# Kernel optimization log

Hardware: AMD Instinct MI355X
Metric: run time of the kernel (lower is better)

Reference implementation:

```python
import jax, jax.numpy as jnp
import numpy as np

D_MODEL = 1024
N_HEADS = 16
D_K = D_MODEL // N_HEADS


def setup_inputs() -> dict:
    key = jax.random.key(0)
    ks = jax.random.split(key, 12)
    B, S = 4, 2048
    scale = 1.0 / np.sqrt(D_MODEL)
    inp = {
        "Q_in": jax.random.normal(ks[0], (B, S, D_MODEL), jnp.float32),
        "K_in": jax.random.normal(ks[1], (B, S, D_MODEL), jnp.float32),
        "V_in": jax.random.normal(ks[2], (B, S, D_MODEL), jnp.float32),
        "Wq": jax.random.normal(ks[3], (D_MODEL, D_MODEL), jnp.float32) * scale,
        "bq": jnp.zeros((D_MODEL,), jnp.float32),
        "Wk": jax.random.normal(ks[4], (D_MODEL, D_MODEL), jnp.float32) * scale,
        "bk": jnp.zeros((D_MODEL,), jnp.float32),
        "Wv": jax.random.normal(ks[5], (D_MODEL, D_MODEL), jnp.float32) * scale,
        "bv": jnp.zeros((D_MODEL,), jnp.float32),
        "Wo": jax.random.normal(ks[6], (D_MODEL, D_MODEL), jnp.float32) * scale,
        "bo": jnp.zeros((D_MODEL,), jnp.float32),
    }
    return inp


def reference(Q_in, K_in, V_in, Wq, bq, Wk, bk, Wv, bv, Wo, bo):
    B, S, _ = Q_in.shape
    # QKV projections, split into heads: [B, H, S, d_k]
    def proj(x, W, b):
        y = jnp.einsum('bsd,df->bsf', x, W) + b
        return y.reshape(B, S, N_HEADS, D_K).transpose(0, 2, 1, 3)

    Q = proj(Q_in, Wq, bq)
    K = proj(K_in, Wk, bk)
    V = proj(V_in, Wv, bv)

    # scaled dot-product attention (dropout is identity in eval)
    scores = jnp.einsum('bhqd,bhkd->bhqk', Q, K) / jnp.sqrt(jnp.float32(D_K)).astype(Q.dtype)
    p_attn = jax.nn.softmax(scores, axis=-1)
    x = jnp.einsum('bhqk,bhkd->bhqd', p_attn, V)

    # merge heads and output projection
    x = x.transpose(0, 2, 1, 3).reshape(B, S, D_MODEL)
    return jnp.einsum('bsd,df->bsf', x, Wo) + bo
```

## Files before the change

kernel.cpp:

```cpp
#include <hip/hip_runtime.h>

#define DEV __device__ __forceinline__

typedef _Float16 f16;
typedef __attribute__((ext_vector_type(8))) _Float16 f16x8;
typedef __attribute__((ext_vector_type(4))) _Float16 f16x4;
typedef __attribute__((ext_vector_type(2))) __fp16 fp16v2;
typedef __attribute__((ext_vector_type(4))) float floatx4;

constexpr int DMODEL = 1024;
constexpr int SLEN = 2048;
constexpr float SCALE_Q = 0.125f * 1.4426950408889634f;

DEV void gll16(const void* g, void* lds) {
    __builtin_amdgcn_global_load_lds((const __attribute__((address_space(1))) void*)g,
                                     (__attribute__((address_space(3))) void*)lds, 16, 0, 0);
}

#if __has_builtin(__builtin_amdgcn_exp2f)
DEV float fast_exp2(float x) { return __builtin_amdgcn_exp2f(x); }
#else
DEV float fast_exp2(float x) { return __expf(x * 0.6931471805599453f); }
#endif

DEV unsigned pkh2(float a, float b) {
    union { fp16v2 h; unsigned u; } c;
    c.h = __builtin_amdgcn_cvt_pkrtz(a, b);
    return c.u;
}

#if __has_builtin(__builtin_amdgcn_permlane32_swap) && __has_builtin(__builtin_amdgcn_permlane16_swap)
DEV void pl32swap(unsigned& x, unsigned& y) {
    auto r = __builtin_amdgcn_permlane32_swap(x, y, false, false);
    x = r[0]; y = r[1];
}
DEV void pl16swap(unsigned& x, unsigned& y) {
    auto r = __builtin_amdgcn_permlane16_swap(x, y, false, false);
    x = r[0]; y = r[1];
}
#else
DEV void pl32swap(unsigned& x, unsigned& y) {
    unsigned xs = (unsigned)__shfl_xor((int)x, 32, 64);
    unsigned ys = (unsigned)__shfl_xor((int)y, 32, 64);
    bool lo = (threadIdx.x & 63) < 32;
    unsigned nx = lo ? x : ys, ny = lo ? xs : y;
    x = nx; y = ny;
}
DEV void pl16swap(unsigned& x, unsigned& y) {
    unsigned xs = (unsigned)__shfl_xor((int)x, 16, 64);
    unsigned ys = (unsigned)__shfl_xor((int)y, 16, 64);
    bool ev = (((threadIdx.x & 63) >> 4) & 1) == 0;
    unsigned nx = ev ? x : ys, ny = ev ? xs : y;
    x = nx; y = ny;
}
#endif

DEV f16x8 xform(const floatx4& s0, const floatx4& s1) {
    unsigned X  = pkh2(fast_exp2(s0[0]), fast_exp2(s0[1]));
    unsigned Xp = pkh2(fast_exp2(s0[2]), fast_exp2(s0[3]));
    unsigned Y  = pkh2(fast_exp2(s1[0]), fast_exp2(s1[1]));
    unsigned Yp = pkh2(fast_exp2(s1[2]), fast_exp2(s1[3]));
    pl32swap(X, Y);  pl16swap(X, Y);
    pl32swap(Xp, Yp); pl16swap(Xp, Yp);
    union { unsigned u[4]; f16x8 v; } o;
    o.u[0] = X; o.u[1] = Xp; o.u[2] = Y; o.u[3] = Yp;
    return o.v;
}

__global__ void cvt3(const float* __restrict__ A0, const float* __restrict__ A1,
                     const float* __restrict__ A2, f16* __restrict__ O0,
                     f16* __restrict__ O1, f16* __restrict__ O2) {
    const int seg = blockIdx.x >> 12;
    const int i = (blockIdx.x & 4095) * 256 + threadIdx.x;
    const float* in = seg == 0 ? A0 : seg == 1 ? A1 : A2;
    f16* out = seg == 0 ? O0 : seg == 1 ? O1 : O2;
    const float4 a = ((const float4*)in)[2 * i];
    const float4 b = ((const float4*)in)[2 * i + 1];
    f16x8 h;
    h[0] = (f16)a.x; h[1] = (f16)a.y; h[2] = (f16)a.z; h[3] = (f16)a.w;
    h[4] = (f16)b.x; h[5] = (f16)b.y; h[6] = (f16)b.z; h[7] = (f16)b.w;
    ((f16x8*)out)[i] = h;
}

__global__ void wtrans4(const float* __restrict__ W0, const float* __restrict__ W1,
                        const float* __restrict__ W2, const float* __restrict__ W3,
                        f16* __restrict__ T0, f16* __restrict__ T1,
                        f16* __restrict__ T2, f16* __restrict__ T3) {
    __shared__ float t[32][33];
    const int w = blockIdx.x >> 10, bid = blockIdx.x & 1023;
    const float* W = w == 0 ? W0 : w == 1 ? W1 : w == 2 ? W2 : W3;
    f16* Wt = w == 0 ? T0 : w == 1 ? T1 : w == 2 ? T2 : T3;
    const int tn = bid & 31, tk = bid >> 5;
    const int c = threadIdx.x & 31, r0 = threadIdx.x >> 5;
    for (int i = 0; i < 4; ++i) {
        int r = r0 + i * 8;
        t[r][c] = W[(tk * 32 + r) * DMODEL + tn * 32 + c];
    }
    __syncthreads();
    for (int i = 0; i < 4; ++i) {
        int r = r0 + i * 8;
        Wt[(tn * 32 + r) * DMODEL + tk * 32 + c] = (f16)t[c][r];
    }
}

__global__ __launch_bounds__(256, 3)
void gemm_qkv(const f16* __restrict__ A0, const f16* __restrict__ A1, const f16* __restrict__ A2,
              const f16* __restrict__ B0, const f16* __restrict__ B1, const f16* __restrict__ B2,
              const float* __restrict__ bi0, const float* __restrict__ bi1, const float* __restrict__ bi2,
              f16* __restrict__ C0, f16* __restrict__ C1, f16* __restrict__ C2, int epi_base) {
    __shared__ f16 As[128 * 32];
    __shared__ f16 Bs[128 * 32];
    const int seg = blockIdx.x >> 9, inner = blockIdx.x & 511;
    const int epi = epi_base + seg;
    const f16* A = seg == 0 ? A0 : seg == 1 ? A1 : A2;
    const f16* Bt = seg == 0 ? B0 : seg == 1 ? B1 : B2;
    const float* bias = seg == 0 ? bi0 : seg == 1 ? bi1 : bi2;
    f16* Cp = seg == 0 ? C0 : seg == 1 ? C1 : C2;

    const int tid = threadIdx.x;
    const int wid = tid >> 6, lane = tid & 63;
    const int quad = lane >> 4, l16 = lane & 15;
    const int bm = inner & 63, bn = inner >> 6;
    const int row0 = bm * 128, col0 = bn * 128;
    const int wm = (wid >> 1) * 64, wn = (wid & 1) * 64;

    floatx4 acc[4][4];
    for (int i = 0; i < 4; ++i)
        for (int j = 0; j < 4; ++j) acc[i][j] = {0.f, 0.f, 0.f, 0.f};

    for (int k0 = 0; k0 < DMODEL; k0 += 32) {
        __syncthreads();
        for (int j = 0; j < 2; ++j) {
            int off = (j * 4 + wid) * 1024 + lane * 16;
            int r = off >> 6, cb = (off & 63) >> 1;
            gll16(Bt + (col0 + r) * DMODEL + k0 + cb, (char*)Bs + (j * 4 + wid) * 1024);
            gll16(A + (row0 + r) * DMODEL + k0 + cb, (char*)As + (j * 4 + wid) * 1024);
        }
        __syncthreads();

        f16x8 af[4], bf[4];
        for (int mi = 0; mi < 4; ++mi)
            af[mi] = *(const f16x8*)&As[(wm + mi * 16 + l16) * 32 + quad * 8];
        for (int ni = 0; ni < 4; ++ni)
            bf[ni] = *(const f16x8*)&Bs[(wn + ni * 16 + l16) * 32 + quad * 8];
        for (int mi = 0; mi < 4; ++mi)
            for (int ni = 0; ni < 4; ++ni)
                acc[mi][ni] = __builtin_amdgcn_mfma_f32_16x16x32_f16(af[mi], bf[ni], acc[mi][ni], 0, 0, 0);
    }

    const float scale = (epi == 0) ? SCALE_Q : 1.0f;
    for (int mi = 0; mi < 4; ++mi) {
        for (int ni = 0; ni < 4; ++ni) {
            const int gr0 = row0 + wm + mi * 16 + quad * 4;
            const int gc = col0 + wn + ni * 16 + l16;
            const float bv = bias[gc];
            if (epi == 2) {
                const int b_ = gr0 >> 11, s0 = gr0 & 2047;
                const int h_ = gc >> 6, d_ = gc & 63;
                const int bh = b_ * 16 + h_;
                const int csw = ((s0 >> 3) & 15) ^ (d_ & 7);
                const int s0w = (s0 & ~127) | (csw << 3) | (s0 & 7);
                f16x4 o;
                for (int r = 0; r < 4; ++r) o[r] = (f16)(acc[mi][ni][r] + bv);
                *(f16x4*)&Cp[(bh * 64 + d_) * SLEN + s0w] = o;
            } else {
                for (int r = 0; r < 4; ++r) {
                    const int gr = gr0 + r;
                    const int b_ = gr >> 11, s_ = gr & 2047;
                    const int h_ = gc >> 6, d_ = gc & 63;
                    const int bh = b_ * 16 + h_;
                    const int dsw = (((d_ >> 3) ^ (s_ & 7)) << 3) | (d_ & 7);
                    Cp[(bh * SLEN + s_) * 64 + dsw] = (f16)((acc[mi][ni][r] + bv) * scale);
                }
            }
        }
    }
}

__global__ __launch_bounds__(256, 3)
void gemm_out(const f16* __restrict__ A, const f16* __restrict__ Bt,
              const float* __restrict__ bias, float* __restrict__ Cp) {
    __shared__ f16 As[128 * 32];
    __shared__ f16 Bs[128 * 32];
    const int tid = threadIdx.x;
    const int wid = tid >> 6, lane = tid & 63;
    const int quad = lane >> 4, l16 = lane & 15;
    const int bm = blockIdx.x & 63, bn = blockIdx.x >> 6;
    const int row0 = bm * 128, col0 = bn * 128;
    const int wm = (wid >> 1) * 64, wn = (wid & 1) * 64;

    floatx4 acc[4][4];
    for (int i = 0; i < 4; ++i)
        for (int j = 0; j < 4; ++j) acc[i][j] = {0.f, 0.f, 0.f, 0.f};

    for (int k0 = 0; k0 < DMODEL; k0 += 32) {
        __syncthreads();
        for (int j = 0; j < 2; ++j) {
            int off = (j * 4 + wid) * 1024 + lane * 16;
            int r = off >> 6, cb = (off & 63) >> 1;
            gll16(Bt + (col0 + r) * DMODEL + k0 + cb, (char*)Bs + (j * 4 + wid) * 1024);
            gll16(A + (row0 + r) * DMODEL + k0 + cb, (char*)As + (j * 4 + wid) * 1024);
        }
        __syncthreads();

        f16x8 af[4], bf[4];
        for (int mi = 0; mi < 4; ++mi)
            af[mi] = *(const f16x8*)&As[(wm + mi * 16 + l16) * 32 + quad * 8];
        for (int ni = 0; ni < 4; ++ni)
            bf[ni] = *(const f16x8*)&Bs[(wn + ni * 16 + l16) * 32 + quad * 8];
        for (int mi = 0; mi < 4; ++mi)
            for (int ni = 0; ni < 4; ++ni)
                acc[mi][ni] = __builtin_amdgcn_mfma_f32_16x16x32_f16(af[mi], bf[ni], acc[mi][ni], 0, 0, 0);
    }

    for (int mi = 0; mi < 4; ++mi)
        for (int ni = 0; ni < 4; ++ni) {
            const int gr0 = row0 + wm + mi * 16 + quad * 4;
            const int gc = col0 + wn + ni * 16 + l16;
            const float bv = bias[gc];
            for (int r = 0; r < 4; ++r)
                Cp[(gr0 + r) * DMODEL + gc] = acc[mi][ni][r] + bv;
        }
}

__global__ __launch_bounds__(256, 4)
void flash_k(const f16* __restrict__ Qh, const f16* __restrict__ Kh,
             const f16* __restrict__ Vt, f16* __restrict__ attn) {
    __shared__ f16 smem[16384];
    f16* Qs = smem;
    f16* Ks = smem;
    f16* Vs = smem + 8192;

    const int tid = threadIdx.x;
    const int wid = tid >> 6, lane = tid & 63;
    const int quad = lane >> 4, l16 = lane & 15;
    const int xcd = blockIdx.x & 7, jj = blockIdx.x >> 3;
    const int bh = xcd * 8 + (jj & 7), qt = jj >> 3;
    const int mq = wid * 32;

    const f16* Qbase = Qh + (bh * SLEN + qt * 128) * 64;
#pragma unroll
    for (int j = 0; j < 4; ++j) {
        const int ch = j * 4 + wid;
        gll16(Qbase + ch * 512 + lane * 8, (char*)Qs + ch * 1024);
    }
    __syncthreads();

    f16x8 qf[2][2];
#pragma unroll
    for (int nq = 0; nq < 2; ++nq)
#pragma unroll
        for (int kc = 0; kc < 2; ++kc)
            qf[nq][kc] = *(const f16x8*)&Qs[(mq + nq * 16 + l16) * 64 +
                                            (((kc * 4 + quad) ^ (l16 & 7)) << 3)];

    floatx4 oacc[2][5];
    for (int nq = 0; nq < 2; ++nq)
        for (int md = 0; md < 5; ++md) oacc[nq][md] = {0.f, 0.f, 0.f, 0.f};

    const f16x8 ones = {(f16)1, (f16)1, (f16)1, (f16)1, (f16)1, (f16)1, (f16)1, (f16)1};
    const f16* Kb = Kh + bh * SLEN * 64;
    const f16* Vb = Vt + bh * 64 * SLEN;

    for (int kv0 = 0; kv0 < SLEN; kv0 += 128) {
        __syncthreads();
#pragma unroll
        for (int j = 0; j < 4; ++j) {
            const int ch = j * 4 + wid;
            gll16(Kb + kv0 * 64 + ch * 512 + lane * 8, (char*)Ks + ch * 1024);
        }
#pragma unroll
        for (int j = 0; j < 4; ++j) {
            const int ch = j * 4 + wid;
            const int ci = ch * 64 + lane;
            const int d_ = ci >> 4, o_ = (ci & 15) * 8;
            gll16(Vb + d_ * SLEN + kv0 + o_, (char*)Vs + ch * 1024);
        }
        __syncthreads();

        f16x8 pf[2];
#pragma unroll
        for (int c = 0; c < 4; ++c) {
            floatx4 sacc[2][2];
            for (int nq = 0; nq < 2; ++nq)
                for (int t = 0; t < 2; ++t) sacc[nq][t] = {0.f, 0.f, 0.f, 0.f};
#pragma unroll
            for (int t = 0; t < 2; ++t) {
                const int a = c * 2 + t;
#pragma unroll
                for (int kc = 0; kc < 2; ++kc) {
                    f16x8 kf = *(const f16x8*)&Ks[(a * 16 + l16) * 64 +
                                                  (((kc * 4 + quad) ^ (l16 & 7)) << 3)];
                    for (int nq = 0; nq < 2; ++nq)
                        sacc[nq][t] = __builtin_amdgcn_mfma_f32_16x16x32_f16(
                            kf, qf[nq][kc], sacc[nq][t], 0, 0, 0);
                }
            }
            if (c > 0) {
                const int cp = c - 1;
#pragma unroll
                for (int md = 0; md < 4; ++md) {
                    f16x8 vf = *(const f16x8*)&Vs[(md * 16 + l16) * 128 +
                                                  (((cp * 4 + quad) ^ (l16 & 7)) << 3)];
                    for (int nq = 0; nq < 2; ++nq)
                        oacc[nq][md] = __builtin_amdgcn_mfma_f32_16x16x32_f16(
                            vf, pf[nq], oacc[nq][md], 0, 0, 0);
                }
                for (int nq = 0; nq < 2; ++nq)
                    oacc[nq][4] = __builtin_amdgcn_mfma_f32_16x16x32_f16(
                        ones, pf[nq], oacc[nq][4], 0, 0, 0);
            }
#pragma unroll
            for (int nq = 0; nq < 2; ++nq) pf[nq] = xform(sacc[nq][0], sacc[nq][1]);
        }
#pragma unroll
        for (int md = 0; md < 4; ++md) {
            f16x8 vf = *(const f16x8*)&Vs[(md * 16 + l16) * 128 +
                                          (((3 * 4 + quad) ^ (l16 & 7)) << 3)];
            for (int nq = 0; nq < 2; ++nq)
                oacc[nq][md] = __builtin_amdgcn_mfma_f32_16x16x32_f16(
                    vf, pf[nq], oacc[nq][md], 0, 0, 0);
        }
        for (int nq = 0; nq < 2; ++nq)
            oacc[nq][4] = __builtin_amdgcn_mfma_f32_16x16x32_f16(
                ones, pf[nq], oacc[nq][4], 0, 0, 0);
    }

    const int b_ = bh >> 4, h_ = bh & 15;
#pragma unroll
    for (int nq = 0; nq < 2; ++nq) {
        const float linv = __frcp_rn(oacc[nq][4][0]);
        const int tok = b_ * SLEN + qt * 128 + mq + nq * 16 + l16;
#pragma unroll
        for (int md = 0; md < 4; ++md) {
            f16x4 o;
            for (int r = 0; r < 4; ++r) o[r] = (f16)(oacc[nq][md][r] * linv);
            *(f16x4*)&attn[tok * DMODEL + h_ * 64 + md * 16 + quad * 4] = o;
        }
    }
}

extern "C" void kernel_launch(void* const* d_in, const int* in_sizes, int n_in,
                              void* d_out, int out_size, void* d_ws, size_t ws_size,
                              hipStream_t stream) {
    (void)in_sizes; (void)n_in; (void)out_size;
    const float* Q_in = (const float*)d_in[0];
    const float* K_in = (const float*)d_in[1];
    const float* V_in = (const float*)d_in[2];
    const float* Wq = (const float*)d_in[3];
    const float* bq = (const float*)d_in[4];
    const float* Wk = (const float*)d_in[5];
    const float* bk = (const float*)d_in[6];
    const float* Wv = (const float*)d_in[7];
    const float* bv = (const float*)d_in[8];
    const float* Wo = (const float*)d_in[9];
    const float* bo = (const float*)d_in[10];
    float* out = (float*)d_out;

    char* ws = (char*)d_ws;
    const size_t MB = 1u << 20;
    f16* wtq = (f16*)(ws + 0 * MB);
    f16* wtk = (f16*)(ws + 2 * MB);
    f16* wtv = (f16*)(ws + 4 * MB);
    f16* wto = (f16*)(ws + 6 * MB);
    f16* Qh  = (f16*)(ws + 8 * MB);
    f16* Kh  = (f16*)(ws + 24 * MB);
    f16* Vt  = (f16*)(ws + 40 * MB);
    f16* At  = (f16*)(ws + 56 * MB);

    wtrans4<<<4096, 256, 0, stream>>>(Wq, Wk, Wv, Wo, wtq, wtk, wtv, wto);

    if (ws_size >= 120 * MB) {
        f16* Ac0 = (f16*)(ws + 72 * MB);
        f16* Ac1 = (f16*)(ws + 88 * MB);
        f16* Ac2 = (f16*)(ws + 104 * MB);
        cvt3<<<3 * 4096, 256, 0, stream>>>(Q_in, K_in, V_in, Ac0, Ac1, Ac2);
        gemm_qkv<<<1536, 256, 0, stream>>>(Ac0, Ac1, Ac2, wtq, wtk, wtv,
                                           bq, bk, bv, Qh, Kh, Vt, 0);
    } else {
        f16* Ac = At;
        cvt3<<<4096, 256, 0, stream>>>(Q_in, Q_in, Q_in, Ac, Ac, Ac);
        gemm_qkv<<<512, 256, 0, stream>>>(Ac, Ac, Ac, wtq, wtq, wtq, bq, bq, bq,
                                          Qh, Qh, Qh, 0);
        cvt3<<<4096, 256, 0, stream>>>(K_in, K_in, K_in, Ac, Ac, Ac);
        gemm_qkv<<<512, 256, 0, stream>>>(Ac, Ac, Ac, wtk, wtk, wtk, bk, bk, bk,
                                          Kh, Kh, Kh, 1);
        cvt3<<<4096, 256, 0, stream>>>(V_in, V_in, V_in, Ac, Ac, Ac);
        gemm_qkv<<<512, 256, 0, stream>>>(Ac, Ac, Ac, wtv, wtv, wtv, bv, bv, bv,
                                          Vt, Vt, Vt, 2);
    }

    flash_k<<<1024, 256, 0, stream>>>(Qh, Kh, Vt, At);
    gemm_out<<<512, 256, 0, stream>>>(At, wto, bo, out);
}
```

Measured before the change: 348.6 us.

## Double-buffer GEMM and flash-attention loads and enlarge attention query tile

Moves the shared GEMM main loop into a helper that double-buffers A/B tiles in LDS, prefetching the next k-slice with global_load_lds while computing on the current one, using vmcnt waits and raw barriers. The flash-attention kernel likewise double-buffers its K/V tiles. It also doubles the query rows per block to 256, with 64 per wave, so each loaded K/V tile is reused across more queries, and it halves the grid. This hides global load latency and cuts K/V traffic, but doubles LDS use and raises register pressure, which lowers occupancy (launch bounds drop to 2) and leaves fewer blocks to spread across the device.

```diff
diff --git a/kernel.cpp b/kernel.cpp
--- a/kernel.cpp
+++ b/kernel.cpp
@@ -103,40 +103,36 @@
     }
 }
 
-__global__ __launch_bounds__(256, 3)
-void gemm_qkv(const f16* __restrict__ A0, const f16* __restrict__ A1, const f16* __restrict__ A2,
-              const f16* __restrict__ B0, const f16* __restrict__ B1, const f16* __restrict__ B2,
-              const float* __restrict__ bi0, const float* __restrict__ bi1, const float* __restrict__ bi2,
-              f16* __restrict__ C0, f16* __restrict__ C1, f16* __restrict__ C2, int epi_base) {
-    __shared__ f16 As[128 * 32];
-    __shared__ f16 Bs[128 * 32];
-    const int seg = blockIdx.x >> 9, inner = blockIdx.x & 511;
-    const int epi = epi_base + seg;
-    const f16* A = seg == 0 ? A0 : seg == 1 ? A1 : A2;
-    const f16* Bt = seg == 0 ? B0 : seg == 1 ? B1 : B2;
-    const float* bias = seg == 0 ? bi0 : seg == 1 ? bi1 : bi2;
-    f16* Cp = seg == 0 ? C0 : seg == 1 ? C1 : C2;
-
-    const int tid = threadIdx.x;
+DEV void gemm_core(const f16* __restrict__ A, const f16* __restrict__ Bt,
+                   f16* smem, int row0, int col0, int tid, floatx4 (&acc)[4][4]) {
     const int wid = tid >> 6, lane = tid & 63;
     const int quad = lane >> 4, l16 = lane & 15;
-    const int bm = inner & 63, bn = inner >> 6;
-    const int row0 = bm * 128, col0 = bn * 128;
     const int wm = (wid >> 1) * 64, wn = (wid & 1) * 64;
-
-    floatx4 acc[4][4];
-    for (int i = 0; i < 4; ++i)
-        for (int j = 0; j < 4; ++j) acc[i][j] = {0.f, 0.f, 0.f, 0.f};
-
-    for (int k0 = 0; k0 < DMODEL; k0 += 32) {
-        __syncthreads();
-        for (int j = 0; j < 2; ++j) {
-            int off = (j * 4 + wid) * 1024 + lane * 16;
-            int r = off >> 6, cb = (off & 63) >> 1;
-            gll16(Bt + (col0 + r) * DMODEL + k0 + cb, (char*)Bs + (j * 4 + wid) * 1024);
-            gll16(A + (row0 + r) * DMODEL + k0 + cb, (char*)As + (j * 4 + wid) * 1024);
-        }
-        __syncthreads();
+    const int off = wid * 1024 + lane * 16;
+    const int r = off >> 6, cb = (off & 63) >> 1;
+
+    {
+        gll16(Bt + (col0 + r) * DMODEL + cb, (char*)(smem + 4096) + wid * 1024);
+        gll16(Bt + (col0 + r + 64) * DMODEL + cb, (char*)(smem + 4096) + 4096 + wid * 1024);
+        gll16(A + (row0 + r) * DMODEL + cb, (char*)smem + wid * 1024);
+        gll16(A + (row0 + r + 64) * DMODEL + cb, (char*)smem + 4096 + wid * 1024);
+    }
+    for (int it = 0; it < 32; ++it) {
+        f16* As = smem + (it & 1) * 8192;
+        f16* Bs = As + 4096;
+        if (it < 31) {
+            const int k0 = (it + 1) * 32;
+            f16* An = smem + ((it + 1) & 1) * 8192;
+            f16* Bn = An + 4096;
+            gll16(Bt + (col0 + r) * DMODEL + k0 + cb, (char*)Bn + wid * 1024);
+            gll16(Bt + (col0 + r + 64) * DMODEL + k0 + cb, (char*)Bn + 4096 + wid * 1024);
+            gll16(A + (row0 + r) * DMODEL + k0 + cb, (char*)An + wid * 1024);
+            gll16(A + (row0 + r + 64) * DMODEL + k0 + cb, (char*)An + 4096 + wid * 1024);
+            __builtin_amdgcn_s_waitcnt(0xF74);
+        } else {
+            __builtin_amdgcn_s_waitcnt(0xF70);
+        }
+        __builtin_amdgcn_s_barrier();
 
         f16x8 af[4], bf[4];
         for (int mi = 0; mi < 4; ++mi)
@@ -146,7 +142,35 @@
         for (int mi = 0; mi < 4; ++mi)
             for (int ni = 0; ni < 4; ++ni)
                 acc[mi][ni] = __builtin_amdgcn_mfma_f32_16x16x32_f16(af[mi], bf[ni], acc[mi][ni], 0, 0, 0);
-    }
+        __builtin_amdgcn_s_barrier();
+    }
+}
+
+__global__ __launch_bounds__(256, 3)
+void gemm_qkv(const f16* __restrict__ A0, const f16* __restrict__ A1, const f16* __restrict__ A2,
+              const f16* __restrict__ B0, const f16* __restrict__ B1, const f16* __restrict__ B2,
+              const float* __restrict__ bi0, const float* __restrict__ bi1, const float* __restrict__ bi2,
+              f16* __restrict__ C0, f16* __restrict__ C1, f16* __restrict__ C2, int epi_base) {
+    __shared__ f16 smem[16384];
+    const int seg = blockIdx.x >> 9, inner = blockIdx.x & 511;
+    const int epi = epi_base + seg;
+    const f16* A = seg == 0 ? A0 : seg == 1 ? A1 : A2;
+    const f16* Bt = seg == 0 ? B0 : seg == 1 ? B1 : B2;
+    const float* bias = seg == 0 ? bi0 : seg == 1 ? bi1 : bi2;
+    f16* Cp = seg == 0 ? C0 : seg == 1 ? C1 : C2;
+
+    const int tid = threadIdx.x;
+    const int wid = tid >> 6, lane = tid & 63;
+    const int quad = lane >> 4, l16 = lane & 15;
+    const int bm = inner & 63, bn = inner >> 6;
+    const int row0 = bm * 128, col0 = bn * 128;
+    const int wm = (wid >> 1) * 64, wn = (wid & 1) * 64;
+
+    floatx4 acc[4][4];
+    for (int i = 0; i < 4; ++i)
+        for (int j = 0; j < 4; ++j) acc[i][j] = {0.f, 0.f, 0.f, 0.f};
+
+    gemm_core(A, Bt, smem, row0, col0, tid, acc);
 
     const float scale = (epi == 0) ? SCALE_Q : 1.0f;
     for (int mi = 0; mi < 4; ++mi) {
@@ -180,8 +204,7 @@
 __global__ __launch_bounds__(256, 3)
 void gemm_out(const f16* __restrict__ A, const f16* __restrict__ Bt,
               const float* __restrict__ bias, float* __restrict__ Cp) {
-    __shared__ f16 As[128 * 32];
-    __shared__ f16 Bs[128 * 32];
+    __shared__ f16 smem[16384];
     const int tid = threadIdx.x;
     const int wid = tid >> 6, lane = tid & 63;
     const int quad = lane >> 4, l16 = lane & 15;
@@ -193,25 +216,7 @@
     for (int i = 0; i < 4; ++i)
         for (int j = 0; j < 4; ++j) acc[i][j] = {0.f, 0.f, 0.f, 0.f};
 
-    for (int k0 = 0; k0 < DMODEL; k0 += 32) {
-        __syncthreads();
-        for (int j = 0; j < 2; ++j) {
-            int off = (j * 4 + wid) * 1024 + lane * 16;
-            int r = off >> 6, cb = (off & 63) >> 1;
-            gll16(Bt + (col0 + r) * DMODEL + k0 + cb, (char*)Bs + (j * 4 + wid) * 1024);
-            gll16(A + (row0 + r) * DMODEL + k0 + cb, (char*)As + (j * 4 + wid) * 1024);
-        }
-        __syncthreads();
-
-        f16x8 af[4], bf[4];
-        for (int mi = 0; mi < 4; ++mi)
-            af[mi] = *(const f16x8*)&As[(wm + mi * 16 + l16) * 32 + quad * 8];
-        for (int ni = 0; ni < 4; ++ni)
-            bf[ni] = *(const f16x8*)&Bs[(wn + ni * 16 + l16) * 32 + quad * 8];
-        for (int mi = 0; mi < 4; ++mi)
-            for (int ni = 0; ni < 4; ++ni)
-                acc[mi][ni] = __builtin_amdgcn_mfma_f32_16x16x32_f16(af[mi], bf[ni], acc[mi][ni], 0, 0, 0);
-    }
+    gemm_core(A, Bt, smem, row0, col0, tid, acc);
 
     for (int mi = 0; mi < 4; ++mi)
         for (int ni = 0; ni < 4; ++ni) {
@@ -223,77 +228,87 @@
         }
 }
 
-__global__ __launch_bounds__(256, 4)
+__global__ __launch_bounds__(256, 2)
 void flash_k(const f16* __restrict__ Qh, const f16* __restrict__ Kh,
              const f16* __restrict__ Vt, f16* __restrict__ attn) {
-    __shared__ f16 smem[16384];
-    f16* Qs = smem;
-    f16* Ks = smem;
-    f16* Vs = smem + 8192;
-
+    __shared__ f16 smem[32768];
     const int tid = threadIdx.x;
     const int wid = tid >> 6, lane = tid & 63;
     const int quad = lane >> 4, l16 = lane & 15;
     const int xcd = blockIdx.x & 7, jj = blockIdx.x >> 3;
     const int bh = xcd * 8 + (jj & 7), qt = jj >> 3;
-    const int mq = wid * 32;
-
-    const f16* Qbase = Qh + (bh * SLEN + qt * 128) * 64;
-#pragma unroll
-    for (int j = 0; j < 4; ++j) {
+    const int wq = wid * 64;
+
+    f16* Qs = smem + 16384;
+    const f16* Qbase = Qh + (bh * SLEN + qt * 256) * 64;
+#pragma unroll
+    for (int j = 0; j < 8; ++j) {
         const int ch = j * 4 + wid;
         gll16(Qbase + ch * 512 + lane * 8, (char*)Qs + ch * 1024);
     }
     __syncthreads();
 
-    f16x8 qf[2][2];
-#pragma unroll
-    for (int nq = 0; nq < 2; ++nq)
+    f16x8 qf[4][2];
+#pragma unroll
+    for (int nq = 0; nq < 4; ++nq)
 #pragma unroll
         for (int kc = 0; kc < 2; ++kc)
-            qf[nq][kc] = *(const f16x8*)&Qs[(mq + nq * 16 + l16) * 64 +
+            qf[nq][kc] = *(const f16x8*)&Qs[(wq + nq * 16 + l16) * 64 +
                                             (((kc * 4 + quad) ^ (l16 & 7)) << 3)];
-
-    floatx4 oacc[2][5];
-    for (int nq = 0; nq < 2; ++nq)
+    __syncthreads();
+
+    floatx4 oacc[4][5];
+    for (int nq = 0; nq < 4; ++nq)
         for (int md = 0; md < 5; ++md) oacc[nq][md] = {0.f, 0.f, 0.f, 0.f};
 
     const f16x8 ones = {(f16)1, (f16)1, (f16)1, (f16)1, (f16)1, (f16)1, (f16)1, (f16)1};
     const f16* Kb = Kh + bh * SLEN * 64;
     const f16* Vb = Vt + bh * 64 * SLEN;
 
-    for (int kv0 = 0; kv0 < SLEN; kv0 += 128) {
-        __syncthreads();
-#pragma unroll
-        for (int j = 0; j < 4; ++j) {
-            const int ch = j * 4 + wid;
-            gll16(Kb + kv0 * 64 + ch * 512 + lane * 8, (char*)Ks + ch * 1024);
-        }
-#pragma unroll
-        for (int j = 0; j < 4; ++j) {
-            const int ch = j * 4 + wid;
-            const int ci = ch * 64 + lane;
-            const int d_ = ci >> 4, o_ = (ci & 15) * 8;
-            gll16(Vb + d_ * SLEN + kv0 + o_, (char*)Vs + ch * 1024);
-        }
-        __syncthreads();
-
-        f16x8 pf[2];
+#pragma unroll
+    for (int j = 0; j < 4; ++j) {
+        const int ch = j * 4 + wid;
+        gll16(Kb + ch * 512 + lane * 8, (char*)smem + ch * 1024);
+        const int ci = ch * 64 + lane;
+        gll16(Vb + (ci >> 4) * SLEN + (ci & 15) * 8, (char*)(smem + 8192) + ch * 1024);
+    }
+
+    for (int t = 0; t < 16; ++t) {
+        f16* Ks = smem + (t & 1) * 16384;
+        f16* Vs = Ks + 8192;
+        if (t < 15) {
+            const int kv0n = (t + 1) * 128;
+            f16* Kn = smem + ((t + 1) & 1) * 16384;
+            f16* Vn = Kn + 8192;
+#pragma unroll
+            for (int j = 0; j < 4; ++j) {
+                const int ch = j * 4 + wid;
+                gll16(Kb + kv0n * 64 + ch * 512 + lane * 8, (char*)Kn + ch * 1024);
+                const int ci = ch * 64 + lane;
+                gll16(Vb + (ci >> 4) * SLEN + kv0n + (ci & 15) * 8, (char*)Vn + ch * 1024);
+            }
+            __builtin_amdgcn_s_waitcnt(0xF78);
+        } else {
+            __builtin_amdgcn_s_waitcnt(0xF70);
+        }
+        __builtin_amdgcn_s_barrier();
+
+        f16x8 pf[4];
 #pragma unroll
         for (int c = 0; c < 4; ++c) {
-            floatx4 sacc[2][2];
-            for (int nq = 0; nq < 2; ++nq)
-                for (int t = 0; t < 2; ++t) sacc[nq][t] = {0.f, 0.f, 0.f, 0.f};
-#pragma unroll
-            for (int t = 0; t < 2; ++t) {
-                const int a = c * 2 + t;
+            floatx4 sacc[4][2];
+            for (int nq = 0; nq < 4; ++nq)
+                for (int t2 = 0; t2 < 2; ++t2) sacc[nq][t2] = {0.f, 0.f, 0.f, 0.f};
+#pragma unroll
+            for (int t2 = 0; t2 < 2; ++t2) {
+                const int a = c * 2 + t2;
 #pragma unroll
                 for (int kc = 0; kc < 2; ++kc) {
                     f16x8 kf = *(const f16x8*)&Ks[(a * 16 + l16) * 64 +
                                                   (((kc * 4 + quad) ^ (l16 & 7)) << 3)];
-                    for (int nq = 0; nq < 2; ++nq)
-                        sacc[nq][t] = __builtin_amdgcn_mfma_f32_16x16x32_f16(
-                            kf, qf[nq][kc], sacc[nq][t], 0, 0, 0);
+                    for (int nq = 0; nq < 4; ++nq)
+                        sacc[nq][t2] = __builtin_amdgcn_mfma_f32_16x16x32_f16(
+                            kf, qf[nq][kc], sacc[nq][t2], 0, 0, 0);
                 }
             }
             if (c > 0) {
@@ -302,35 +317,37 @@
                 for (int md = 0; md < 4; ++md) {
                     f16x8 vf = *(const f16x8*)&Vs[(md * 16 + l16) * 128 +
                                                   (((cp * 4 + quad) ^ (l16 & 7)) << 3)];
-                    for (int nq = 0; nq < 2; ++nq)
+                    for (int nq = 0; nq < 4; ++nq)
                         oacc[nq][md] = __builtin_amdgcn_mfma_f32_16x16x32_f16(
                             vf, pf[nq], oacc[nq][md], 0, 0, 0);
                 }
-                for (int nq = 0; nq < 2; ++nq)
+                for (int nq = 0; nq < 4; ++nq)
                     oacc[nq][4] = __builtin_amdgcn_mfma_f32_16x16x32_f16(
                         ones, pf[nq], oacc[nq][4], 0, 0, 0);
             }
 #pragma unroll
-            for (int nq = 0; nq < 2; ++nq) pf[nq] = xform(sacc[nq][0], sacc[nq][1]);
+            for (int nq = 0; nq < 4; ++nq) pf[nq] = xform(sacc[nq][0], sacc[nq][1]);
         }
 #pragma unroll
         for (int md = 0; md < 4; ++md) {
             f16x8 vf = *(const f16x8*)&Vs[(md * 16 + l16) * 128 +
                                           (((3 * 4 + quad) ^ (l16 & 7)) << 3)];
-            for (int nq = 0; nq < 2; ++nq)
+            for (int nq = 0; nq < 4; ++nq)
                 oacc[nq][md] = __builtin_amdgcn_mfma_f32_16x16x32_f16(
                     vf, pf[nq], oacc[nq][md], 0, 0, 0);
         }
-        for (int nq = 0; nq < 2; ++nq)
+        for (int nq = 0; nq < 4; ++nq)
             oacc[nq][4] = __builtin_amdgcn_mfma_f32_16x16x32_f16(
                 ones, pf[nq], oacc[nq][4], 0, 0, 0);
+
+        __builtin_amdgcn_s_barrier();
     }
 
     const int b_ = bh >> 4, h_ = bh & 15;
 #pragma unroll
-    for (int nq = 0; nq < 2; ++nq) {
+    for (int nq = 0; nq < 4; ++nq) {
         const float linv = __frcp_rn(oacc[nq][4][0]);
-        const int tok = b_ * SLEN + qt * 128 + mq + nq * 16 + l16;
+        const int tok = b_ * SLEN + qt * 256 + wq + nq * 16 + l16;
 #pragma unroll
         for (int md = 0; md < 4; ++md) {
             f16x4 o;
@@ -390,6 +407,6 @@
                                           Vt, Vt, Vt, 2);
     }
 
-    flash_k<<<1024, 256, 0, stream>>>(Qh, Kh, Vt, At);
+    flash_k<<<512, 256, 0, stream>>>(Qh, Kh, Vt, At);
     gemm_out<<<512, 256, 0, stream>>>(At, wto, bo, out);
 }
```

New measurement: 323.7 us. -7.1%, faster.
